# Performance work log

Hardware: AMD Instinct MI355X
Metric: run time of the kernel (lower is better)

## Reference

```python
import jax, jax.numpy as jnp
import numpy as np

EMBED = 1024
HEADS = 16
HEAD_DIM = EMBED // HEADS
SCALE = HEAD_DIM ** -0.5


def setup_inputs() -> dict:
    key = jax.random.key(0)
    ks = jax.random.split(key, 11)
    B, S, D = 2, 2048, EMBED
    s = D ** -0.5
    return {
        "Q": jax.random.normal(ks[0], (B, S, D), jnp.float32),
        "K": jax.random.normal(ks[1], (B, S, D), jnp.float32),
        "V": jax.random.normal(ks[2], (B, S, D), jnp.float32),
        "Wq": jax.random.normal(ks[3], (D, D), jnp.float32) * s,
        "bq": jax.random.normal(ks[4], (D,), jnp.float32) * 0.01,
        "Wk": jax.random.normal(ks[5], (D, D), jnp.float32) * s,
        "bk": jax.random.normal(ks[6], (D,), jnp.float32) * 0.01,
        "Wv": jax.random.normal(ks[7], (D, D), jnp.float32) * s,
        "bv": jax.random.normal(ks[8], (D,), jnp.float32) * 0.01,
        "Wo": jax.random.normal(ks[9], (D, D), jnp.float32) * s,
        "bo": jax.random.normal(ks[10], (D,), jnp.float32) * 0.01,
    }


def reference(Q, K, V, Wq, bq, Wk, bk, Wv, bv, Wo, bo):
    N, S, D = Q.shape
    H, Hd = HEADS, HEAD_DIM
    # linear projections (x @ W + b), then split heads: [N, S, H, Hd]
    q = (Q @ Wq + bq).reshape(N, S, H, Hd)
    k = (K @ Wk + bk).reshape(N, S, H, Hd)
    v = (V @ Wv + bv).reshape(N, S, H, Hd)
    # scaled dot-product attention, full [N,H,S,S] scores as in the original
    energy = jnp.einsum('nqhd,nkhd->nhqk', q, k) * SCALE
    attn = jax.nn.softmax(energy, axis=3)
    out = jnp.einsum('nhql,nlhd->nqhd', attn, v).reshape(N, S, D)
    return out @ Wo + bo
```

## Files before the change

### kernel.cpp

```cpp
#include <hip/hip_runtime.h>
#include <cstdint>


typedef _Float16 h8 __attribute__((ext_vector_type(8)));
typedef float f4 __attribute__((ext_vector_type(4)));
typedef float f16v __attribute__((ext_vector_type(16)));
typedef unsigned int u32x4 __attribute__((ext_vector_type(4)));
typedef const unsigned int __attribute__((address_space(1)))* gp1_t;
typedef unsigned int __attribute__((address_space(3)))* lp3_t;

#define FSWZ(r) ((((r) ^ ((r) >> 3))) & 7)

__device__ __forceinline__ void gld_lds16(const void* g, const void* l) {
  __builtin_amdgcn_global_load_lds((gp1_t)(uintptr_t)g,
                                   (lp3_t)(unsigned int)(uintptr_t)l, 16, 0, 0);
}
__device__ __forceinline__ unsigned pkh(float a, float b) {
  return __builtin_bit_cast(unsigned, __builtin_amdgcn_cvt_pkrtz(a, b));
}
__device__ __forceinline__ void plswap(unsigned& a, unsigned& b) {
  asm volatile("v_permlane32_swap_b32 %0, %1" : "+v"(a), "+v"(b));
}


__global__ void cvt_w4(const float* __restrict__ wq, const float* __restrict__ wk,
                       const float* __restrict__ wv, const float* __restrict__ wo,
                       _Float16* __restrict__ WT) {
  const int z = blockIdx.z;
  const float* W = (z == 0) ? wq : (z == 1) ? wk : (z == 2) ? wv : wo;
  _Float16* o = WT + (size_t)z * 1048576;
  const int k = blockIdx.x * 256 + threadIdx.x;
  const int n0 = blockIdx.y * 4;
  float4 w = *(const float4*)(W + (size_t)k * 1024 + n0);
  o[(size_t)(n0 + 0) * 1024 + k] = (_Float16)w.x;
  o[(size_t)(n0 + 1) * 1024 + k] = (_Float16)w.y;
  o[(size_t)(n0 + 2) * 1024 + k] = (_Float16)w.z;
  o[(size_t)(n0 + 3) * 1024 + k] = (_Float16)w.w;
}


#define A_LOAD(KT)                                                             \
  do {                                                                         \
    _Pragma("unroll") for (int i_ = 0; i_ < 4; ++i_) {                         \
      const int idx_ = i_ * 256 + tid;                                         \
      const int r_ = idx_ >> 3, g_ = idx_ & 7;                                 \
      const float* ap_ = A32 + (size_t)(row0 + r_) * 1024 + (KT) * 64 + g_ * 8;\
      fa[i_] = *(const float4*)ap_;                                            \
      fb[i_] = *(const float4*)(ap_ + 4);                                      \
    }                                                                          \
  } while (0)

#define A_WRITE(BUF)                                                           \
  do {                                                                         \
    _Pragma("unroll") for (int i_ = 0; i_ < 4; ++i_) {                         \
      const int idx_ = i_ * 256 + tid;                                         \
      const int r_ = idx_ >> 3, g_ = idx_ & 7;                                 \
      u32x4 w_ = {pkh(fa[i_].x, fa[i_].y), pkh(fa[i_].z, fa[i_].w),            \
                  pkh(fb[i_].x, fb[i_].y), pkh(fb[i_].z, fb[i_].w)};           \
      *(u32x4*)&As[BUF][r_ * 64 + ((g_ ^ FSWZ(r_)) << 3)] = w_;                \
    }                                                                          \
  } while (0)

#define B_STAGE(BUF, KT)                                                       \
  do {                                                                         \
    _Pragma("unroll") for (int rr_ = 0; rr_ < 4; ++rr_) {                      \
      const int idx_ = rr_ * 256 + tid;                                        \
      const int r_ = idx_ >> 3, g_ = idx_ & 7;                                 \
      gld_lds16(Bt + (size_t)(col0 + r_) * 1024 + (KT) * 64 + (g_ ^ FSWZ(r_)) * 8,\
                &Bs[BUF][(rr_ * 256 + wave * 64) * 8]);                        \
    }                                                                          \
  } while (0)

__global__ __launch_bounds__(256, 2) void gemm_qkv(const float* __restrict__ Qf,
                                                   const float* __restrict__ Kf,
                                                   const float* __restrict__ Vf,
                                                   const _Float16* __restrict__ WT,
                                                   const float* __restrict__ bq,
                                                   const float* __restrict__ bk,
                                                   const float* __restrict__ bv,
                                                   _Float16* __restrict__ qkv16) {
  __shared__ _Float16 As[2][8192];
  __shared__ _Float16 Bs[2][8192];
  const int z = blockIdx.z;
  const float* A32 = (z == 0) ? Qf : (z == 1) ? Kf : Vf;
  const _Float16* Bt = WT + (size_t)z * 1048576;
  const float* bias = (z == 0) ? bq : (z == 1) ? bk : bv;
  _Float16* out16 = qkv16 + (size_t)z * 4194304;
  const float scl = (z == 0) ? 0.18033688f : 1.0f;
  const int tid = threadIdx.x;
  const int wave = tid >> 6, lane = tid & 63;
  const int lg = lane >> 4, ll = lane & 15;
  const int wr = wave >> 1, wc = wave & 1;
  const int row0 = blockIdx.x * 128, col0 = blockIdx.y * 128;
  f4 acc[4][4] = {};
  float4 fa[4], fb[4];
  A_LOAD(0);
  B_STAGE(0, 0);
  A_WRITE(0);
  __syncthreads();
  int cur = 0;
  for (int kt = 0; kt < 16; ++kt) {
    const bool pre = (kt + 1 < 16);
    if (pre) { A_LOAD(kt + 1); B_STAGE(cur ^ 1, kt + 1); }
#pragma unroll
    for (int kk = 0; kk < 2; ++kk) {
      h8 af[4], bf[4];
#pragma unroll
      for (int mi = 0; mi < 4; ++mi) {
        const int r = wr * 64 + mi * 16 + ll;
        af[mi] = *(const h8*)&As[cur][r * 64 + (((kk * 4 + lg) ^ FSWZ(r)) << 3)];
      }
#pragma unroll
      for (int ni = 0; ni < 4; ++ni) {
        const int r = wc * 64 + ni * 16 + ll;
        bf[ni] = *(const h8*)&Bs[cur][r * 64 + (((kk * 4 + lg) ^ FSWZ(r)) << 3)];
      }
#pragma unroll
      for (int mi = 0; mi < 4; ++mi)
#pragma unroll
        for (int ni = 0; ni < 4; ++ni)
          acc[mi][ni] = __builtin_amdgcn_mfma_f32_16x16x32_f16(af[mi], bf[ni],
                                                               acc[mi][ni], 0, 0, 0);
    }
    if (pre) A_WRITE(cur ^ 1);
    __syncthreads();
    cur ^= 1;
  }
#pragma unroll
  for (int ni = 0; ni < 4; ++ni) {
    const int c = col0 + wc * 64 + ni * 16 + ll;
    const float bv = bias[c];
#pragma unroll
    for (int mi = 0; mi < 4; ++mi) {
#pragma unroll
      for (int i = 0; i < 4; ++i) {
        const int r = row0 + wr * 64 + mi * 16 + lg * 4 + i;
        const float val = (acc[mi][ni][i] + bv) * scl;
        const int b = r >> 11, s = r & 2047, h = c >> 6, hd = c & 63;
        out16[((size_t)((b * 16 + h) * 2048 + s)) * 64 + hd] = (_Float16)val;
      }
    }
  }
}


#define GO_STAGE(BUF, KT)                                                      \
  do {                                                                         \
    _Pragma("unroll") for (int rr_ = 0; rr_ < 4; ++rr_) {                      \
      const int idx_ = rr_ * 256 + tid;                                        \
      const int r_ = idx_ >> 3, g_ = idx_ & 7;                                 \
      gld_lds16(A16 + (size_t)(row0 + r_) * 1024 + (KT) * 64 + (g_ ^ FSWZ(r_)) * 8,\
                &As[BUF][(rr_ * 256 + wave * 64) * 8]);                        \
    }                                                                          \
    _Pragma("unroll") for (int rr_ = 0; rr_ < 2; ++rr_) {                      \
      const int idx_ = rr_ * 256 + tid;                                        \
      const int r_ = idx_ >> 3, g_ = idx_ & 7;                                 \
      gld_lds16(WoT + (size_t)(col0 + r_) * 1024 + (KT) * 64 + (g_ ^ FSWZ(r_)) * 8,\
                &Bs[BUF][(rr_ * 256 + wave * 64) * 8]);                        \
    }                                                                          \
  } while (0)

__global__ __launch_bounds__(256, 2) void gemm_out_k(const _Float16* __restrict__ A16,
                                                     const _Float16* __restrict__ WoT,
                                                     const float* __restrict__ bo,
                                                     float* __restrict__ out) {
  __shared__ _Float16 As[2][8192];
  __shared__ _Float16 Bs[2][4096];
  const int tid = threadIdx.x;
  const int wave = tid >> 6, lane = tid & 63;
  const int lg = lane >> 4, ll = lane & 15;
  const int wr = wave >> 1, wc = wave & 1;
  const int row0 = blockIdx.x * 128, col0 = blockIdx.y * 64;
  f4 acc[4][2] = {};
  GO_STAGE(0, 0);
  __syncthreads();
  int cur = 0;
  for (int kt = 0; kt < 16; ++kt) {
    if (kt + 1 < 16) GO_STAGE(cur ^ 1, kt + 1);
#pragma unroll
    for (int kk = 0; kk < 2; ++kk) {
      h8 af[4], bf[2];
#pragma unroll
      for (int mi = 0; mi < 4; ++mi) {
        const int r = wr * 64 + mi * 16 + ll;
        af[mi] = *(const h8*)&As[cur][r * 64 + (((kk * 4 + lg) ^ FSWZ(r)) << 3)];
      }
#pragma unroll
      for (int ni = 0; ni < 2; ++ni) {
        const int r = wc * 32 + ni * 16 + ll;
        bf[ni] = *(const h8*)&Bs[cur][r * 64 + (((kk * 4 + lg) ^ FSWZ(r)) << 3)];
      }
#pragma unroll
      for (int mi = 0; mi < 4; ++mi)
#pragma unroll
        for (int ni = 0; ni < 2; ++ni)
          acc[mi][ni] = __builtin_amdgcn_mfma_f32_16x16x32_f16(af[mi], bf[ni],
                                                               acc[mi][ni], 0, 0, 0);
    }
    __syncthreads();
    cur ^= 1;
  }
#pragma unroll
  for (int ni = 0; ni < 2; ++ni) {
    const int c = col0 + wc * 32 + ni * 16 + ll;
    const float bv = bo[c];
#pragma unroll
    for (int mi = 0; mi < 4; ++mi)
#pragma unroll
      for (int i = 0; i < 4; ++i) {
        const int r = row0 + wr * 64 + mi * 16 + lg * 4 + i;
        out[(size_t)r * 1024 + c] = acc[mi][ni][i] + bv;
      }
  }
}


#define STAGE_K(BUF, KT)                                                      \
  do {                                                                        \
    _Pragma("unroll") for (int rr_ = 0; rr_ < 2; ++rr_) {                     \
      const int idx_ = rr_ * 256 + tid;                                       \
      const int r_ = idx_ >> 3, g_ = idx_ & 7;                                \
      gld_lds16(kbp + (size_t)((KT) * 64 + r_) * 64 + ((g_ ^ FSWZ(r_)) * 8),  \
                &Ks[BUF][(rr_ * 256 + wave * 64) * 8]);                       \
    }                                                                         \
  } while (0)

#define LOAD_V(KT)                                                            \
  do {                                                                        \
    const _Float16* vp_ = vbp + (size_t)((KT) * 64 + vkey0) * 64 + vhd0;      \
    va = *(const uint4*)vp_;                                                  \
    vc = *(const uint4*)(vp_ + 64);                                           \
  } while (0)

#define WRITE_V(BUF)                                                          \
  do {                                                                        \
    const unsigned short* pa_ = (const unsigned short*)&va;                   \
    const unsigned short* pc_ = (const unsigned short*)&vc;                   \
    _Pragma("unroll") for (int j_ = 0; j_ < 8; ++j_) {                        \
      const int row_ = vhd0 + j_;                                             \
      *(unsigned*)&Vt[BUF][row_ * 64 + (((vkey0 >> 3) ^ FSWZ(row_)) << 3) +   \
                           (vkey0 & 7)] =                                     \
          (unsigned)pa_[j_] | ((unsigned)pc_[j_] << 16);                      \
    }                                                                         \
  } while (0)

#define QK_COMPUTE(BUF, S0, S1)                                               \
  do {                                                                        \
    S0 = (f16v){};                                                            \
    S1 = (f16v){};                                                            \
    _Pragma("unroll") for (int kc_ = 0; kc_ < 4; ++kc_) {                     \
      const int c_ = kc_ * 2 + hi;                                            \
      h8 k0_ = *(const h8*)&Ks[BUF][l31 * 64 + ((c_ ^ FSWZ(l31)) << 3)];      \
      h8 k1_ = *(const h8*)&Ks[BUF][(32 + l31) * 64 +                         \
                                    ((c_ ^ FSWZ(32 + l31)) << 3)];            \
      h8 qf_ = (kc_ == 0) ? qf0 : (kc_ == 1) ? qf1 : (kc_ == 2) ? qf2 : qf3;  \
      S0 = __builtin_amdgcn_mfma_f32_32x32x16_f16(k0_, qf_, S0, 0, 0, 0);     \
      S1 = __builtin_amdgcn_mfma_f32_32x32x16_f16(k1_, qf_, S1, 0, 0, 0);     \
    }                                                                         \
  } while (0)

#define PACK_AF(DST, SX, PP)                                                  \
  do {                                                                        \
    unsigned wA = pkh(SX[(PP) + 0], SX[(PP) + 1]);                            \
    unsigned wB = pkh(SX[(PP) + 2], SX[(PP) + 3]);                            \
    unsigned wC = pkh(SX[(PP) + 4], SX[(PP) + 5]);                            \
    unsigned wD = pkh(SX[(PP) + 6], SX[(PP) + 7]);                            \
    plswap(wA, wC);                                                           \
    plswap(wB, wD);                                                           \
    DST = (u32x4){wA, wB, wC, wD};                                            \
  } while (0)

#define SM_PK(S0, S1)                                                         \
  do {                                                                        \
    float t_[8];                                                              \
    _Pragma("unroll") for (int j2_ = 0; j2_ < 8; ++j2_)                       \
        t_[j2_] = fmaxf(fmaxf(S0[j2_], S0[j2_ + 8]),                          \
                        fmaxf(S1[j2_], S1[j2_ + 8]));                         \
    float pm_ = fmaxf(fmaxf(fmaxf(t_[0], t_[1]), fmaxf(t_[2], t_[3])),        \
                      fmaxf(fmaxf(t_[4], t_[5]), fmaxf(t_[6], t_[7])));       \
    pm_ = fmaxf(pm_, __shfl_xor(pm_, 32));                                    \
    if (__any(pm_ > mval + 8.0f)) {                                           \
      const float mn_ = fmaxf(mval, pm_);                                     \
      const float f_ = __builtin_amdgcn_exp2f(mval - mn_);                    \
      mval = mn_;                                                             \
      lsum *= f_;                                                             \
      Fb[wave][l31] = f_;                                                     \
      const f4 fr0_ = *(const f4*)&Fb[wave][0 + 4 * hi];                      \
      const f4 fr1_ = *(const f4*)&Fb[wave][8 + 4 * hi];                      \
      const f4 fr2_ = *(const f4*)&Fb[wave][16 + 4 * hi];                     \
      const f4 fr3_ = *(const f4*)&Fb[wave][24 + 4 * hi];                     \
      _Pragma("unroll") for (int r_ = 0; r_ < 16; ++r_) {                     \
        const float fx_ =                                                     \
            (r_ < 4 ? fr0_ : r_ < 8 ? fr1_ : r_ < 12 ? fr2_ : fr3_)[r_ & 3];  \
        acc0[r_] *= fx_;                                                      \
        acc1[r_] *= fx_;                                                      \
      }                                                                       \
    }                                                                         \
    _Pragma("unroll") for (int r_ = 0; r_ < 16; ++r_) {                       \
      S0[r_] = __builtin_amdgcn_exp2f(S0[r_] - mval);                         \
      S1[r_] = __builtin_amdgcn_exp2f(S1[r_] - mval);                         \
    }                                                                         \
    float z_[8];                                                              \
    _Pragma("unroll") for (int j2_ = 0; j2_ < 8; ++j2_)                       \
        z_[j2_] = (S0[j2_] + S0[j2_ + 8]) + (S1[j2_] + S1[j2_ + 8]);          \
    lsum += ((z_[0] + z_[1]) + (z_[2] + z_[3])) +                             \
            ((z_[4] + z_[5]) + (z_[6] + z_[7]));                              \
    PACK_AF(afr[0], S0, 0);                                                   \
    PACK_AF(afr[1], S0, 8);                                                   \
    PACK_AF(afr[2], S1, 0);                                                   \
    PACK_AF(afr[3], S1, 8);                                                   \
  } while (0)

#define PV_APPLY(BUF)                                                         \
  do {                                                                        \
    _Pragma("unroll") for (int i_ = 0; i_ < 4; ++i_) {                        \
      const int c_ = i_ * 2 + hi;                                             \
      h8 vf0_ = *(const h8*)&Vt[BUF][l31 * 64 + ((c_ ^ FSWZ(l31)) << 3)];     \
      h8 vf1_ = *(const h8*)&Vt[BUF][(32 + l31) * 64 +                        \
                                     ((c_ ^ FSWZ(32 + l31)) << 3)];           \
      h8 af_ = __builtin_bit_cast(h8, afr[i_]);                               \
      acc0 = __builtin_amdgcn_mfma_f32_32x32x16_f16(af_, vf0_, acc0, 0, 0, 0);\
      acc1 = __builtin_amdgcn_mfma_f32_32x32x16_f16(af_, vf1_, acc1, 0, 0, 0);\
    }                                                                         \
  } while (0)

__global__ __launch_bounds__(256, 2) void attn_kernel(
    const _Float16* __restrict__ q16, const _Float16* __restrict__ k16,
    const _Float16* __restrict__ v16, _Float16* __restrict__ aout) {
  __shared__ _Float16 Ks[2][4096];
  __shared__ _Float16 Vt[2][4096];
  __shared__ float Fb[4][32];
  const int tid = threadIdx.x;
  const int wave = tid >> 6, lane = tid & 63;
  const int l31 = lane & 31, hi = lane >> 5;
  const int blk = blockIdx.x;
  const int xcd = blk & 7, j = blk >> 3;
  const int bh = xcd * 4 + (j >> 4);
  const int qb = j & 15;
  const int q0w = qb * 128 + wave * 32;
  const _Float16* qbp = q16 + (size_t)bh * 131072;
  const _Float16* kbp = k16 + (size_t)bh * 131072;
  const _Float16* vbp = v16 + (size_t)bh * 131072;
  const int vkey0 = (tid & 31) * 2, vhd0 = (tid >> 5) * 8;

  h8 qf0 = *(const h8*)(qbp + (size_t)(q0w + l31) * 64 + 0 + hi * 8);
  h8 qf1 = *(const h8*)(qbp + (size_t)(q0w + l31) * 64 + 16 + hi * 8);
  h8 qf2 = *(const h8*)(qbp + (size_t)(q0w + l31) * 64 + 32 + hi * 8);
  h8 qf3 = *(const h8*)(qbp + (size_t)(q0w + l31) * 64 + 48 + hi * 8);

  f16v acc0 = {}, acc1 = {};
  f16v sr0 = {}, sr1 = {};
  u32x4 afr[4];
  float mval = -1e30f, lsum = 0.f;
  uint4 va, vc;

  STAGE_K(0, 0);
  LOAD_V(0);
  WRITE_V(0);
  __syncthreads();
  QK_COMPUTE(0, sr0, sr1);
  STAGE_K(1, 1);
  LOAD_V(1);
  WRITE_V(1);
  SM_PK(sr0, sr1);
  __syncthreads();

  for (int t = 0; t < 31; ++t) {
    const int A = t & 1, B = A ^ 1;
    if (t + 2 < 32) LOAD_V(t + 2);
    __builtin_amdgcn_s_setprio(1);
    QK_COMPUTE(B, sr0, sr1);
    PV_APPLY(A);
    __builtin_amdgcn_s_setprio(0);
    __builtin_amdgcn_sched_barrier(0);
    __syncthreads();
    if (t + 2 < 32) { STAGE_K(A, t + 2); WRITE_V(A); }
    SM_PK(sr0, sr1);
    __syncthreads();
  }
  PV_APPLY(1);

  lsum += __shfl_xor(lsum, 32);
  const float inv = 1.0f / lsum;
  Fb[wave][l31] = inv;
  const f4 ir0 = *(const f4*)&Fb[wave][0 + 4 * hi];
  const f4 ir1 = *(const f4*)&Fb[wave][8 + 4 * hi];
  const f4 ir2 = *(const f4*)&Fb[wave][16 + 4 * hi];
  const f4 ir3 = *(const f4*)&Fb[wave][24 + 4 * hi];
  const int b = bh >> 4, h = bh & 15;
#pragma unroll
  for (int r = 0; r < 16; ++r) {
    const float fx = (r < 4 ? ir0 : r < 8 ? ir1 : r < 12 ? ir2 : ir3)[r & 3];
    const int srow = q0w + (r & 3) + 8 * (r >> 2) + 4 * hi;
    _Float16* op = aout + ((size_t)(b * 2048 + srow)) * 1024 + h * 64 + l31;
    op[0] = (_Float16)(acc0[r] * fx);
    op[32] = (_Float16)(acc1[r] * fx);
  }
}


extern "C" void kernel_launch(void* const* d_in, const int* in_sizes, int n_in,
                              void* d_out, int out_size, void* d_ws, size_t ws_size,
                              hipStream_t stream) {
  const float* Q  = (const float*)d_in[0];
  const float* K  = (const float*)d_in[1];
  const float* V  = (const float*)d_in[2];
  const float* Wq = (const float*)d_in[3];
  const float* bq = (const float*)d_in[4];
  const float* Wk = (const float*)d_in[5];
  const float* bk = (const float*)d_in[6];
  const float* Wv = (const float*)d_in[7];
  const float* bv = (const float*)d_in[8];
  const float* Wo = (const float*)d_in[9];
  const float* bo = (const float*)d_in[10];

  _Float16* H      = (_Float16*)d_ws;
  _Float16* WT     = H + 12582912;
  _Float16* qkv16  = H + 16777216;
  _Float16* aout16 = H + 29360128;
  float* out = (float*)d_out;

  cvt_w4<<<dim3(4, 256, 4), 256, 0, stream>>>(Wq, Wk, Wv, Wo, WT);
  gemm_qkv<<<dim3(32, 8, 3), 256, 0, stream>>>(Q, K, V, WT, bq, bk, bv, qkv16);
  attn_kernel<<<dim3(512), 256, 0, stream>>>(qkv16, qkv16 + 4194304,
                                             qkv16 + 8388608, aout16);
  gemm_out_k<<<dim3(32, 16), 256, 0, stream>>>(aout16, WT + 3145728, bo, out);
}
```

Measured before the change: 125.0 us.

## Pre-convert Q/K/V to fp16 and stage both GEMM operands via global-to-LDS loads

Adds a separate kernel that converts the fp32 Q, K and V activations to fp16 in workspace. The QKV projection GEMM can then load its A operand straight into LDS with global_load_lds, like the B operand, instead of doing register loads, packing and LDS writes. This drops the register-staged path and its VGPR pressure, at the cost of an extra kernel launch and a full read/write pass over 3x4M elements. Separately, the output GEMM's launch bounds are raised to 3 blocks per CU.

```diff
diff --git a/kernel.cpp b/kernel.cpp
--- a/kernel.cpp
+++ b/kernel.cpp
@@ -22,6 +22,19 @@
   asm volatile("v_permlane32_swap_b32 %0, %1" : "+v"(a), "+v"(b));
 }
 
+
+__global__ void cvt_x3(const float* __restrict__ a, const float* __restrict__ b,
+                       const float* __restrict__ c, _Float16* __restrict__ out) {
+  const int z = blockIdx.z;
+  const float* in = (z == 0) ? a : (z == 1) ? b : c;
+  _Float16* o = out + (size_t)z * 4194304;
+  const int i = (blockIdx.x * 256 + threadIdx.x) * 8;
+  float4 u = *(const float4*)(in + i);
+  float4 w = *(const float4*)(in + i + 4);
+  h8 r = {(_Float16)u.x, (_Float16)u.y, (_Float16)u.z, (_Float16)u.w,
+          (_Float16)w.x, (_Float16)w.y, (_Float16)w.z, (_Float16)w.w};
+  *(h8*)(o + i) = r;
+}
 
 __global__ void cvt_w4(const float* __restrict__ wq, const float* __restrict__ wk,
                        const float* __restrict__ wv, const float* __restrict__ wo,
@@ -39,41 +52,20 @@
 }
 
 
-#define A_LOAD(KT)                                                             \
-  do {                                                                         \
-    _Pragma("unroll") for (int i_ = 0; i_ < 4; ++i_) {                         \
-      const int idx_ = i_ * 256 + tid;                                         \
-      const int r_ = idx_ >> 3, g_ = idx_ & 7;                                 \
-      const float* ap_ = A32 + (size_t)(row0 + r_) * 1024 + (KT) * 64 + g_ * 8;\
-      fa[i_] = *(const float4*)ap_;                                            \
-      fb[i_] = *(const float4*)(ap_ + 4);                                      \
-    }                                                                          \
-  } while (0)
-
-#define A_WRITE(BUF)                                                           \
-  do {                                                                         \
-    _Pragma("unroll") for (int i_ = 0; i_ < 4; ++i_) {                         \
-      const int idx_ = i_ * 256 + tid;                                         \
-      const int r_ = idx_ >> 3, g_ = idx_ & 7;                                 \
-      u32x4 w_ = {pkh(fa[i_].x, fa[i_].y), pkh(fa[i_].z, fa[i_].w),            \
-                  pkh(fb[i_].x, fb[i_].y), pkh(fb[i_].z, fb[i_].w)};           \
-      *(u32x4*)&As[BUF][r_ * 64 + ((g_ ^ FSWZ(r_)) << 3)] = w_;                \
-    }                                                                          \
-  } while (0)
-
-#define B_STAGE(BUF, KT)                                                       \
+#define G_STAGE(BUF, KT)                                                       \
   do {                                                                         \
     _Pragma("unroll") for (int rr_ = 0; rr_ < 4; ++rr_) {                      \
       const int idx_ = rr_ * 256 + tid;                                        \
       const int r_ = idx_ >> 3, g_ = idx_ & 7;                                 \
+      const int lb_ = (rr_ * 256 + wave * 64) * 8;                             \
+      gld_lds16(A16 + (size_t)(row0 + r_) * 1024 + (KT) * 64 + (g_ ^ FSWZ(r_)) * 8,\
+                &As[BUF][lb_]);                                                \
       gld_lds16(Bt + (size_t)(col0 + r_) * 1024 + (KT) * 64 + (g_ ^ FSWZ(r_)) * 8,\
-                &Bs[BUF][(rr_ * 256 + wave * 64) * 8]);                        \
+                &Bs[BUF][lb_]);                                                \
     }                                                                          \
   } while (0)
 
-__global__ __launch_bounds__(256, 2) void gemm_qkv(const float* __restrict__ Qf,
-                                                   const float* __restrict__ Kf,
-                                                   const float* __restrict__ Vf,
+__global__ __launch_bounds__(256, 2) void gemm_qkv(const _Float16* __restrict__ X16,
                                                    const _Float16* __restrict__ WT,
                                                    const float* __restrict__ bq,
                                                    const float* __restrict__ bk,
@@ -82,7 +74,7 @@
   __shared__ _Float16 As[2][8192];
   __shared__ _Float16 Bs[2][8192];
   const int z = blockIdx.z;
-  const float* A32 = (z == 0) ? Qf : (z == 1) ? Kf : Vf;
+  const _Float16* A16 = X16 + (size_t)z * 4194304;
   const _Float16* Bt = WT + (size_t)z * 1048576;
   const float* bias = (z == 0) ? bq : (z == 1) ? bk : bv;
   _Float16* out16 = qkv16 + (size_t)z * 4194304;
@@ -93,15 +85,11 @@
   const int wr = wave >> 1, wc = wave & 1;
   const int row0 = blockIdx.x * 128, col0 = blockIdx.y * 128;
   f4 acc[4][4] = {};
-  float4 fa[4], fb[4];
-  A_LOAD(0);
-  B_STAGE(0, 0);
-  A_WRITE(0);
+  G_STAGE(0, 0);
   __syncthreads();
   int cur = 0;
   for (int kt = 0; kt < 16; ++kt) {
-    const bool pre = (kt + 1 < 16);
-    if (pre) { A_LOAD(kt + 1); B_STAGE(cur ^ 1, kt + 1); }
+    if (kt + 1 < 16) G_STAGE(cur ^ 1, kt + 1);
 #pragma unroll
     for (int kk = 0; kk < 2; ++kk) {
       h8 af[4], bf[4];
@@ -122,7 +110,6 @@
           acc[mi][ni] = __builtin_amdgcn_mfma_f32_16x16x32_f16(af[mi], bf[ni],
                                                                acc[mi][ni], 0, 0, 0);
     }
-    if (pre) A_WRITE(cur ^ 1);
     __syncthreads();
     cur ^= 1;
   }
@@ -160,7 +147,7 @@
     }                                                                          \
   } while (0)
 
-__global__ __launch_bounds__(256, 2) void gemm_out_k(const _Float16* __restrict__ A16,
+__global__ __launch_bounds__(256, 3) void gemm_out_k(const _Float16* __restrict__ A16,
                                                      const _Float16* __restrict__ WoT,
                                                      const float* __restrict__ bo,
                                                      float* __restrict__ out) {
@@ -415,13 +402,15 @@
   const float* bo = (const float*)d_in[10];
 
   _Float16* H      = (_Float16*)d_ws;
+  _Float16* X16    = H;
   _Float16* WT     = H + 12582912;
   _Float16* qkv16  = H + 16777216;
   _Float16* aout16 = H + 29360128;
   float* out = (float*)d_out;
 
+  cvt_x3<<<dim3(2048, 1, 3), 256, 0, stream>>>(Q, K, V, X16);
   cvt_w4<<<dim3(4, 256, 4), 256, 0, stream>>>(Wq, Wk, Wv, Wo, WT);
-  gemm_qkv<<<dim3(32, 8, 3), 256, 0, stream>>>(Q, K, V, WT, bq, bk, bv, qkv16);
+  gemm_qkv<<<dim3(32, 8, 3), 256, 0, stream>>>(X16, WT, bq, bk, bv, qkv16);
   attn_kernel<<<dim3(512), 256, 0, stream>>>(qkv16, qkv16 + 4194304,
                                              qkv16 + 8388608, aout16);
   gemm_out_k<<<dim3(32, 16), 256, 0, stream>>>(aout16, WT + 3145728, bo, out);
```

Result: slower. 129.5 us (+3.6%).
